# Performance work log

Hardware: AMD Instinct MI355X
Metric: run time of the kernel (lower is better)

The kernel has to match this reference:

```python
import jax, jax.numpy as jnp
import numpy as np

B, T, C = 8, 2048, 1024
HS = 128           # head_size
N_TERMS = 2
THETA = 10000.0


def _rope_tables(dim, end):
    freqs = 1.0 / (THETA ** (jnp.arange(0, dim, 2, dtype=jnp.float32) / dim))  # [dim/2]
    ang = jnp.arange(end, dtype=jnp.float32)[:, None] * freqs[None, :]          # [end, dim/2]
    return jnp.cos(ang), jnp.sin(ang)


def _apply_rope(x, cos, sin):
    # x: [..., T, D]; pairs are interleaved (x0,x1),(x2,x3),...
    xr = x[..., 0::2]
    xi = x[..., 1::2]
    or_ = xr * cos - xi * sin
    oi = xr * sin + xi * cos
    return jnp.stack([or_, oi], axis=-1).reshape(x.shape)


def setup_inputs() -> dict:
    key = jax.random.key(0)
    ks = jax.random.split(key, 6)
    x = jax.random.normal(ks[0], (B, T, C), dtype=jnp.float32)
    Wq = jax.random.normal(ks[1], (N_TERMS, C, HS), dtype=jnp.float32) * 0.02
    Wk = jax.random.normal(ks[2], (N_TERMS, C, HS), dtype=jnp.float32) * 0.02
    Wv = jax.random.normal(ks[3], (C, 2 * HS), dtype=jnp.float32) * 0.02
    lambda_q = jax.random.normal(ks[4], (N_TERMS, HS), dtype=jnp.float32) * 0.1
    lambda_k = jax.random.normal(ks[5], (N_TERMS, HS), dtype=jnp.float32) * 0.1
    return {"x": x, "Wq": Wq, "Wk": Wk, "Wv": Wv,
            "lambda_q": lambda_q, "lambda_k": lambda_k, "layer_idx": 3}


def reference(x, Wq, Wk, Wv, lambda_q, lambda_k, layer_idx):
    Bx, Tx, Cx = x.shape
    n = Wq.shape[0]
    scale = 1.0 / (HS ** 0.5)

    v = x @ Wv                                   # [B,T,2*HS]
    q = jnp.einsum('btc,ncd->nbtd', x, Wq)       # [n,B,T,HS]
    k = jnp.einsum('btc,ncd->nbtd', x, Wk)

    cos, sin = _rope_tables(HS, Tx)              # [T, HS/2]
    q = _apply_rope(q, cos, sin)
    k = _apply_rope(k, cos, sin)

    att = jnp.einsum('nbtd,nbsd->nbts', q, k) * scale  # [n,B,T,T]
    causal = jnp.tril(jnp.ones((Tx, Tx), dtype=bool))
    att = jnp.where(causal, att, -jnp.inf)
    att = jax.nn.softmax(att, axis=-1)

    # lambda values
    lam_init = 0.8 - 0.6 * jnp.exp(-0.3 * (jnp.float32(layer_idx) - 1.0))
    e = jnp.mean(jnp.exp(lambda_q * lambda_k), axis=-1)         # [n]
    e_prev = jnp.concatenate([jnp.zeros((1,), e.dtype), e[:-1]])
    lam = e - e_prev + lam_init                                 # [n]
    signs = jnp.where(jnp.arange(n) % 2 == 1, -1.0, 1.0)

    diff_att = jnp.einsum('n,nbts->bts', signs * lam, att)      # [B,T,T]
    out = diff_att @ v                                          # [B,T,2*HS]
    return out
```

## Files before the change

### kernel.cpp

```cpp
#include <hip/hip_runtime.h>
#include <math.h>

#define B_DIM 8
#define T_DIM 2048
#define C_DIM 1024
#define HS_DIM 128
#define VD 256
#define M_DIM (B_DIM * T_DIM)
#define QK_ELEMS (M_DIM * HS_DIM)
#define SCALE 0.088388347648318447f
#define LOG_THETA 9.210340371976184f

#define QB_OFF   0u
#define KB_OFF   4194304u
#define VT_OFF   8388608u
#define WT_OFF   12582912u
#define XBH_OFF  13369344u
#define LAM_OFF  21757952u
#define XSPLIT_ELEMS 8388608u

typedef short s8v   __attribute__((ext_vector_type(8)));
typedef float f32x4 __attribute__((ext_vector_type(4)));
typedef float f32x16 __attribute__((ext_vector_type(16)));

__device__ __forceinline__ unsigned int bf16_rne(float f) {
    unsigned int u = __float_as_uint(f);
    return (u + 0x7fffu + ((u >> 16) & 1u)) >> 16;
}
__device__ __forceinline__ unsigned int pack_bf2(float lo, float hi) {
    return bf16_rne(lo) | (bf16_rne(hi) << 16);
}
__device__ __forceinline__ void async_cp16(const unsigned short* g, unsigned short* l) {
    __builtin_amdgcn_global_load_lds(
        (const __attribute__((address_space(1))) unsigned int*)g,
        (__attribute__((address_space(3))) unsigned int*)l, 16, 0, 0);
}

__global__ __launch_bounds__(256) void prep_kernel(
    const float* __restrict__ x,
    const float* __restrict__ Wq, const float* __restrict__ Wk,
    const float* __restrict__ Wv,
    const float* __restrict__ lq, const float* __restrict__ lk,
    const int* __restrict__ lidx,
    unsigned short* __restrict__ xlo, unsigned short* __restrict__ xhi,
    unsigned short* __restrict__ wt, float* __restrict__ lam_out) {
    __shared__ float tile[32][33];
    const int bx = blockIdx.x;
    const int t = threadIdx.x;

    if (bx < 8192) {
        const size_t i8 = ((size_t)bx * 256 + t) * 8;
        float4 a = *(const float4*)(x + i8);
        float4 b = *(const float4*)(x + i8 + 4);
        uint4 u;
        u.x = pack_bf2(a.x, a.y); u.y = pack_bf2(a.z, a.w);
        u.z = pack_bf2(b.x, b.y); u.w = pack_bf2(b.z, b.w);
        unsigned short* dst = (i8 < XSPLIT_ELEMS) ? (xlo + i8) : (xhi + (i8 - XSPLIT_ELEMS));
        *(uint4*)dst = u;
    } else if (bx < 8960) {
        const int bxx = bx - 8192;
        const int n0 = (bxx % 24) * 32;
        const int k0 = (bxx / 24) * 32;
        const int seg = n0 >> 7;
        const int nl = t & 31;
        const int ng = n0 + nl;
        const int ngl = ng & 127;
        const int pcol = 2 * ((ngl & 15) + ((ngl >> 5) << 4)) + ((ngl >> 4) & 1);
        const float* src; int ld;
        if (seg < 2)      { src = Wq + (size_t)seg * (C_DIM * HS_DIM) + pcol; ld = 128; }
        else if (seg < 4) { src = Wk + (size_t)(seg - 2) * (C_DIM * HS_DIM) + pcol; ld = 128; }
        else              { src = Wv + (ng - 512); ld = 256; }
        #pragma unroll
        for (int rep = 0; rep < 4; ++rep) {
            int kl = (t >> 5) + rep * 8;
            tile[kl][nl] = src[(size_t)(k0 + kl) * ld];
        }
        __syncthreads();
        unsigned int* wt32 = (unsigned int*)wt;
        #pragma unroll
        for (int rep = 0; rep < 2; ++rep) {
            int nl2 = (t >> 4) + rep * 16;
            int k2 = (t & 15) * 2;
            unsigned int u = pack_bf2(tile[k2][nl2], tile[k2 + 1][nl2]);
            wt32[((size_t)(n0 + nl2) * 1024 + k0 + k2) >> 1] = u;
        }
    } else {
        if (t < 64) {
            float s0 = expf(lq[t] * lk[t]) + expf(lq[t + 64] * lk[t + 64]);
            float s1 = expf(lq[128 + t] * lk[128 + t]) + expf(lq[192 + t] * lk[192 + t]);
            #pragma unroll
            for (int off = 32; off > 0; off >>= 1) {
                s0 += __shfl_down(s0, off);
                s1 += __shfl_down(s1, off);
            }
            if (t == 0) {
                float e0 = s0 * (1.0f / 128.0f);
                float e1 = s1 * (1.0f / 128.0f);
                float li = 0.8f - 0.6f * expf(-0.3f * ((float)lidx[0] - 1.0f));
                lam_out[0] = e0 + li;
                lam_out[1] = -(e1 - e0 + li);
            }
        }
    }
}

__global__ __launch_bounds__(256) void gemm_kernel(
    const unsigned short* __restrict__ xlo, const unsigned short* __restrict__ xhi,
    const unsigned short* __restrict__ wt,
    unsigned short* __restrict__ qo, unsigned short* __restrict__ ko,
    unsigned short* __restrict__ vo) {
    __shared__ unsigned short AB[2][2][128 * 64];

    const int t = threadIdx.x;
    const int wv = t >> 6, lane = t & 63;
    const int quad = lane >> 4, l15 = lane & 15;
    const int m0 = blockIdx.x * 128;
    const int n0 = blockIdx.y * 128;
    const int wr = wv >> 1, wc = wv & 1;

    const unsigned short* xbase = (m0 < 8192)
        ? (xlo + (size_t)m0 * C_DIM) : (xhi + (size_t)(m0 - 8192) * C_DIM);
    const unsigned short* wbase = wt + (size_t)n0 * C_DIM;

    f32x4 acc[4][4];
    #pragma unroll
    for (int i = 0; i < 4; ++i)
        #pragma unroll
        for (int j = 0; j < 4; ++j) acc[i][j] = (f32x4){0.f, 0.f, 0.f, 0.f};

    int srow[4], sco[4];
    #pragma unroll
    for (int rep = 0; rep < 4; ++rep) {
        const int ci = t + rep * 256;
        srow[rep] = ci >> 3;
        sco[rep] = ((ci & 7) ^ (srow[rep] & 7)) * 8;
    }

    #pragma unroll
    for (int rep = 0; rep < 4; ++rep) {
        const int ci = t + rep * 256;
        async_cp16(xbase + (size_t)srow[rep] * C_DIM + sco[rep], &AB[0][0][ci * 8]);
        async_cp16(wbase + (size_t)srow[rep] * C_DIM + sco[rep], &AB[0][1][ci * 8]);
    }

    for (int it = 0; it < 16; ++it) {
        const int cur = it & 1;
        asm volatile("s_waitcnt vmcnt(0)" ::: "memory");
        __builtin_amdgcn_s_barrier();
        if (it + 1 < 16) {
            const int kn = (it + 1) * 64;
            #pragma unroll
            for (int rep = 0; rep < 4; ++rep) {
                const int ci = t + rep * 256;
                async_cp16(xbase + (size_t)srow[rep] * C_DIM + kn + sco[rep],
                           &AB[cur ^ 1][0][ci * 8]);
                async_cp16(wbase + (size_t)srow[rep] * C_DIM + kn + sco[rep],
                           &AB[cur ^ 1][1][ci * 8]);
            }
        }
        const unsigned short* As = AB[cur][0];
        const unsigned short* Bs = AB[cur][1];
        #pragma unroll
        for (int kk = 0; kk < 2; ++kk) {
            s8v af[4], bf[4];
            #pragma unroll
            for (int i = 0; i < 4; ++i) {
                const int row = wr * 64 + i * 16 + l15;
                const int xch = (kk * 4 + quad) ^ (row & 7);
                af[i] = *(const s8v*)&As[row * 64 + xch * 8];
            }
            #pragma unroll
            for (int j = 0; j < 4; ++j) {
                const int row = wc * 64 + j * 16 + l15;
                const int xch = (kk * 4 + quad) ^ (row & 7);
                bf[j] = *(const s8v*)&Bs[row * 64 + xch * 8];
            }
            #pragma unroll
            for (int i = 0; i < 4; ++i)
                #pragma unroll
                for (int j = 0; j < 4; ++j)
                    acc[i][j] = __builtin_amdgcn_mfma_f32_16x16x32_bf16(af[i], bf[j], acc[i][j], 0, 0, 0);
        }
    }

    const int seg = n0 >> 7;
    if (seg < 4) {
        unsigned short* dstbuf = ((seg < 2) ? qo : ko) + (size_t)(seg & 1) * QK_ELEMS;
        const int mi0 = l15 + 32 * wc;
        const int mi1 = mi0 + 16;
        const float freq0 = __expf((float)mi0 * (-LOG_THETA / 64.f));
        const float freq1 = __expf((float)mi1 * (-LOG_THETA / 64.f));
        #pragma unroll
        for (int i = 0; i < 4; ++i) {
            #pragma unroll
            for (int e = 0; e < 4; ++e) {
                const int m = m0 + wr * 64 + i * 16 + quad * 4 + e;
                const float trow = (float)(m & (T_DIM - 1));
                unsigned int* p32 = (unsigned int*)(dstbuf + (size_t)m * HS_DIM);
                float sn0, cs0, sn1, cs1;
                __sincosf(trow * freq0, &sn0, &cs0);
                __sincosf(trow * freq1, &sn1, &cs1);
                const float xr0 = acc[i][0][e], xi0 = acc[i][1][e];
                const float xr1 = acc[i][2][e], xi1 = acc[i][3][e];
                p32[mi0] = pack_bf2(xr0 * cs0 - xi0 * sn0, xr0 * sn0 + xi0 * cs0);
                p32[mi1] = pack_bf2(xr1 * cs1 - xi1 * sn1, xr1 * sn1 + xi1 * cs1);
            }
        }
    } else {
        const int bq = m0 >> 11;
        const int tbase = m0 & (T_DIM - 1);
        unsigned int* vT32 = (unsigned int*)vo;
        #pragma unroll
        for (int j = 0; j < 4; ++j) {
            const int d = (seg - 4) * 128 + wc * 64 + j * 16 + l15;
            const size_t rowbase = (size_t)(bq * VD + d) * (T_DIM / 2);
            #pragma unroll
            for (int i = 0; i < 4; ++i) {
                const int tok = tbase + wr * 64 + i * 16 + quad * 4;
                uint2 u;
                u.x = pack_bf2(acc[i][j][0], acc[i][j][1]);
                u.y = pack_bf2(acc[i][j][2], acc[i][j][3]);
                *(uint2*)&vT32[rowbase + (tok >> 1)] = u;
            }
        }
    }
}

#define PSTR 72
#define OSTR 260
#define BUFB 65536
#define P_OFF 131072
#define PSZ  9216
#define SM_TOTAL 149504

__global__ __launch_bounds__(512, 1) void attn_kernel(
    const unsigned short* __restrict__ qg, const unsigned short* __restrict__ kg,
    const unsigned short* __restrict__ vg, const float* __restrict__ lam,
    float* __restrict__ outp) {
    __shared__ __align__(16) unsigned char smem[SM_TOTAL];

    const int t = threadIdx.x;
    const int id = blockIdx.x;
    const int b = id & 7;
    const int kp = id >> 3;

    const int w = t >> 6, lane = t & 63;
    const int l31 = lane & 31, lh = lane >> 5;
    const int sg = w >> 2;
    const int term = w & 1;
    const int kh = (w >> 1) & 1;

    const int strip = sg ? kp : (63 - kp);
    const int q0 = strip * 32;
    const int ntS = (strip >> 1) + 1;
    const int ntB = ((63 - kp) >> 1) + 1;

    unsigned short* Ps = (unsigned short*)(smem + P_OFF + sg * PSZ);
    float* Lsum = (float*)(smem + P_OFF + sg * PSZ);
    float* Ol = (float*)(smem + sg * BUFB);

    const float cn = lam[term];

    const unsigned short* qrow = qg
        + ((size_t)(term * B_DIM + b) * T_DIM + q0 + l31) * HS_DIM + lh * 8;
    s8v qa[8];
    #pragma unroll
    for (int ks = 0; ks < 8; ++ks)
        qa[ks] = *(const s8v*)(qrow + ks * 16);

    unsigned int kOffA[4], vOffA[4];
    #pragma unroll
    for (int rep = 0; rep < 4; ++rep) {
        const int c = t + rep * 512;
        const int rowg = c >> 4, slot = c & 15;
        const int kterm = rowg >> 6, krow = rowg & 63;
        const int kss = slot ^ (krow & 15);
        kOffA[rep] = (unsigned int)(((kterm * B_DIM + b) * T_DIM + krow) * HS_DIM
                                    + kss * 8);
        const int drow = rowg;
        const int vss = slot ^ (drow & 15);
        const int dim = 2 * drow + (vss >> 3), tokc = vss & 7;
        vOffA[rep] = (unsigned int)((b * VD + dim) * T_DIM + tokc * 8);
    }

    f32x16 o[4];
    #pragma unroll
    for (int dt = 0; dt < 4; ++dt)
        #pragma unroll
        for (int r = 0; r < 16; ++r) o[dt][r] = 0.f;
    float l_acc[16];
    #pragma unroll
    for (int r = 0; r < 16; ++r) l_acc[r] = 0.f;

    {
        unsigned short* kb0 = (unsigned short*)(smem + w * 1024);
        unsigned short* vb0 = (unsigned short*)(smem + 32768 + w * 1024);
        #pragma unroll
        for (int rep = 0; rep < 4; ++rep) {
            async_cp16(kg + kOffA[rep], kb0 + rep * 4096);
            async_cp16(vg + vOffA[rep], vb0 + rep * 4096);
        }
    }
    __syncthreads();

    const int krow = kh * 32 + l31;
    const int k15 = l31 & 15;

    for (int it = 0; it < ntB; ++it) {
        const int s0 = it * 64;
        const unsigned char* buf = smem + (it & 1) * BUFB;

        if (it + 1 < ntB) {
            const int sn = s0 + 64;
            unsigned char* nbuf = smem + ((it + 1) & 1) * BUFB;
            unsigned short* kbn = (unsigned short*)(nbuf + w * 1024);
            unsigned short* vbn = (unsigned short*)(nbuf + 32768 + w * 1024);
            #pragma unroll
            for (int rep = 0; rep < 4; ++rep) {
                async_cp16(kg + kOffA[rep] + (size_t)sn * HS_DIM, kbn + rep * 4096);
                async_cp16(vg + vOffA[rep] + sn, vbn + rep * 4096);
            }
        }

        if (it < ntS) {
            const unsigned short* Kb = (const unsigned short*)buf;
            f32x16 sc;
            #pragma unroll
            for (int r = 0; r < 16; ++r) sc[r] = 0.f;
            __builtin_amdgcn_s_setprio(1);
            #pragma unroll
            for (int ks = 0; ks < 8; ++ks) {
                const int x = (ks * 2 + lh) ^ k15;
                s8v kf = *(const s8v*)&Kb[(term * 64 + krow) * 128 + x * 8];
                sc = __builtin_amdgcn_mfma_f32_32x32x16_bf16(qa[ks], kf, sc, 0, 0, 0);
            }
            __builtin_amdgcn_s_setprio(0);
            const int key = s0 + kh * 32 + l31;
            #pragma unroll
            for (int r = 0; r < 16; ++r) {
                const int row = (r & 3) + 8 * (r >> 2) + 4 * lh;
                const float p = (key <= q0 + row) ? __expf(sc[r] * SCALE) : 0.f;
                l_acc[r] += p;
                Ps[(term * 32 + row) * PSTR + kh * 32 + l31] = (unsigned short)bf16_rne(p);
            }
        }
        asm volatile("s_waitcnt lgkmcnt(0)\n\ts_barrier" ::: "memory");
        __builtin_amdgcn_sched_barrier(0);

        if (it < ntS) {
            const unsigned short* Vb = (const unsigned short*)(buf + 32768);
            __builtin_amdgcn_s_setprio(1);
            #pragma unroll
            for (int ks = 0; ks < 4; ++ks) {
                s8v pa = *(const s8v*)&Ps[(term * 32 + l31) * PSTR + ks * 16 + lh * 8];
                #pragma unroll
                for (int dt = 0; dt < 4; ++dt) {
                    const int dim = kh * 128 + dt * 32 + l31;
                    const int drow = dim >> 1;
                    const int x = ((dim & 1) * 8 + ks * 2 + lh) ^ (drow & 15);
                    s8v vb = *(const s8v*)&Vb[(drow * 16 + x) * 8];
                    o[dt] = __builtin_amdgcn_mfma_f32_32x32x16_bf16(pa, vb, o[dt], 0, 0, 0);
                }
            }
            __builtin_amdgcn_s_setprio(0);
        }
        __syncthreads();
    }

    #pragma unroll
    for (int r = 0; r < 16; ++r) {
        float lt = l_acc[r];
        #pragma unroll
        for (int off = 1; off < 32; off <<= 1) lt += __shfl_xor(lt, off);
        if (l31 == 0) {
            const int row = (r & 3) + 8 * (r >> 2) + 4 * lh;
            Lsum[(term * 2 + kh) * 32 + row] = lt;
        }
    }
    __syncthreads();
    float inv[16];
    #pragma unroll
    for (int r = 0; r < 16; ++r) {
        const int row = (r & 3) + 8 * (r >> 2) + 4 * lh;
        inv[r] = cn / (Lsum[(term * 2 + 0) * 32 + row] + Lsum[(term * 2 + 1) * 32 + row]);
    }

    if (term) {
        #pragma unroll
        for (int dt = 0; dt < 4; ++dt)
            #pragma unroll
            for (int r = 0; r < 16; ++r) {
                const int row = (r & 3) + 8 * (r >> 2) + 4 * lh;
                Ol[row * OSTR + kh * 128 + dt * 32 + l31] = o[dt][r] * inv[r];
            }
    }
    __syncthreads();
    if (!term) {
        #pragma unroll
        for (int dt = 0; dt < 4; ++dt)
            #pragma unroll
            for (int r = 0; r < 16; ++r) {
                const int row = (r & 3) + 8 * (r >> 2) + 4 * lh;
                Ol[row * OSTR + kh * 128 + dt * 32 + l31] += o[dt][r] * inv[r];
            }
    }
    __syncthreads();
    #pragma unroll
    for (int rep = 0; rep < 8; ++rep) {
        int idx = (t & 255) + rep * 256;
        int row = idx >> 6, c4 = idx & 63;
        float4 val = *(const float4*)&Ol[row * OSTR + c4 * 4];
        *(float4*)&outp[((size_t)(b * T_DIM + q0 + row)) * VD + c4 * 4] = val;
    }
}

extern "C" void kernel_launch(void* const* d_in, const int* in_sizes, int n_in,
                              void* d_out, int out_size, void* d_ws, size_t ws_size,
                              hipStream_t stream) {
    const float* x  = (const float*)d_in[0];
    const float* Wq = (const float*)d_in[1];
    const float* Wk = (const float*)d_in[2];
    const float* Wv = (const float*)d_in[3];
    const float* lq = (const float*)d_in[4];
    const float* lk = (const float*)d_in[5];
    const int* lidx = (const int*)d_in[6];

    unsigned short* ws = (unsigned short*)d_ws;
    unsigned short* qb   = ws + QB_OFF;
    unsigned short* kb   = ws + KB_OFF;
    unsigned short* vTb  = ws + VT_OFF;
    unsigned short* wtb  = ws + WT_OFF;
    unsigned short* xbhi = ws + XBH_OFF;
    float* lamb = (float*)(ws + LAM_OFF);
    unsigned short* xblo = (unsigned short*)d_out;
    (void)ws_size; (void)in_sizes; (void)n_in; (void)out_size;

    prep_kernel<<<dim3(8961), dim3(256), 0, stream>>>(
        x, Wq, Wk, Wv, lq, lk, lidx, xblo, xbhi, wtb, lamb);
    gemm_kernel<<<dim3(128, 6), dim3(256), 0, stream>>>(xblo, xbhi, wtb, qb, kb, vTb);
    attn_kernel<<<dim3(256), dim3(512), 0, stream>>>(qb, kb, vTb, lamb, (float*)d_out);
}
```

Measured before the change: 200.5 us.

## Fuse prep, projection GEMM and attention into one persistent kernel with grid barriers

Replaces the three launches (prep, GEMM, attention) with a single persistent 256-block kernel. Phases are separated by software grid barriers built on an atomic counter that is cleared with a memset before launch. The intent is to remove launch gaps and tail effects between the kernels. In exchange, the GEMM now runs as 512 half-block tiles in two rounds, with some tiles left idle. Correctness also depends on all 256 blocks being resident at once, since otherwise the spin barrier can deadlock.

```diff
diff --git a/kernel.cpp b/kernel.cpp
--- a/kernel.cpp
+++ b/kernel.cpp
@@ -17,11 +17,19 @@
 #define WT_OFF   12582912u
 #define XBH_OFF  13369344u
 #define LAM_OFF  21757952u
+#define BAR_OFF  21757960u
 #define XSPLIT_ELEMS 8388608u
 
 typedef short s8v   __attribute__((ext_vector_type(8)));
 typedef float f32x4 __attribute__((ext_vector_type(4)));
 typedef float f32x16 __attribute__((ext_vector_type(16)));
+
+#define PSTR 72
+#define OSTR 260
+#define BUFB 65536
+#define P_OFF 131072
+#define PSZ  9216
+#define SM_TOTAL 149504
 
 __device__ __forceinline__ unsigned int bf16_rne(float f) {
     unsigned int u = __float_as_uint(f);
@@ -35,382 +43,400 @@
         (const __attribute__((address_space(1))) unsigned int*)g,
         (__attribute__((address_space(3))) unsigned int*)l, 16, 0, 0);
 }
-
-__global__ __launch_bounds__(256) void prep_kernel(
+__device__ __forceinline__ void grid_barrier(unsigned int* ctr) {
+    __syncthreads();
+    if (threadIdx.x == 0) {
+        __atomic_fetch_add(ctr, 1u, __ATOMIC_ACQ_REL);
+        while (__atomic_load_n(ctr, __ATOMIC_ACQUIRE) < 256u)
+            __builtin_amdgcn_s_sleep(16);
+    }
+    __syncthreads();
+}
+
+__global__ __launch_bounds__(512, 1) void mega_kernel(
     const float* __restrict__ x,
     const float* __restrict__ Wq, const float* __restrict__ Wk,
     const float* __restrict__ Wv,
     const float* __restrict__ lq, const float* __restrict__ lk,
     const int* __restrict__ lidx,
     unsigned short* __restrict__ xlo, unsigned short* __restrict__ xhi,
-    unsigned short* __restrict__ wt, float* __restrict__ lam_out) {
-    __shared__ float tile[32][33];
-    const int bx = blockIdx.x;
+    unsigned short* __restrict__ wt, float* __restrict__ lamb,
+    unsigned short* __restrict__ qb, unsigned short* __restrict__ kb,
+    unsigned short* __restrict__ vT, float* __restrict__ outp,
+    unsigned int* __restrict__ bar) {
+    __shared__ __align__(16) unsigned char smem[SM_TOTAL];
+
     const int t = threadIdx.x;
-
-    if (bx < 8192) {
-        const size_t i8 = ((size_t)bx * 256 + t) * 8;
-        float4 a = *(const float4*)(x + i8);
-        float4 b = *(const float4*)(x + i8 + 4);
-        uint4 u;
-        u.x = pack_bf2(a.x, a.y); u.y = pack_bf2(a.z, a.w);
-        u.z = pack_bf2(b.x, b.y); u.w = pack_bf2(b.z, b.w);
-        unsigned short* dst = (i8 < XSPLIT_ELEMS) ? (xlo + i8) : (xhi + (i8 - XSPLIT_ELEMS));
-        *(uint4*)dst = u;
-    } else if (bx < 8960) {
-        const int bxx = bx - 8192;
-        const int n0 = (bxx % 24) * 32;
-        const int k0 = (bxx / 24) * 32;
-        const int seg = n0 >> 7;
-        const int nl = t & 31;
-        const int ng = n0 + nl;
-        const int ngl = ng & 127;
-        const int pcol = 2 * ((ngl & 15) + ((ngl >> 5) << 4)) + ((ngl >> 4) & 1);
-        const float* src; int ld;
-        if (seg < 2)      { src = Wq + (size_t)seg * (C_DIM * HS_DIM) + pcol; ld = 128; }
-        else if (seg < 4) { src = Wk + (size_t)(seg - 2) * (C_DIM * HS_DIM) + pcol; ld = 128; }
-        else              { src = Wv + (ng - 512); ld = 256; }
+    const int bid = blockIdx.x;
+
+    {
+        const int idx = bid * 512 + t;
+        #pragma unroll 4
+        for (int iter = 0; iter < 16; ++iter) {
+            const size_t i8 = (size_t)(idx + (iter << 17)) * 8;
+            float4 a = *(const float4*)(x + i8);
+            float4 b = *(const float4*)(x + i8 + 4);
+            uint4 u;
+            u.x = pack_bf2(a.x, a.y); u.y = pack_bf2(a.z, a.w);
+            u.z = pack_bf2(b.x, b.y); u.w = pack_bf2(b.z, b.w);
+            unsigned short* dst = (i8 < XSPLIT_ELEMS) ? (xlo + i8)
+                                                      : (xhi + (i8 - XSPLIT_ELEMS));
+            *(uint4*)dst = u;
+        }
+    }
+    {
+        float (*tile)[33] = (float(*)[33])smem;
+        for (int r = 0; r < 3; ++r) {
+            const int bxx = bid + (r << 8);
+            const int n0 = (bxx % 24) * 32;
+            const int k0 = (bxx / 24) * 32;
+            const int seg = n0 >> 7;
+            const int nl = t & 31;
+            const int ng = n0 + nl;
+            const int ngl = ng & 127;
+            const int pcol = 2 * ((ngl & 15) + ((ngl >> 5) << 4)) + ((ngl >> 4) & 1);
+            const float* src; int ld;
+            if (seg < 2)      { src = Wq + (size_t)seg * (C_DIM * HS_DIM) + pcol; ld = 128; }
+            else if (seg < 4) { src = Wk + (size_t)(seg - 2) * (C_DIM * HS_DIM) + pcol; ld = 128; }
+            else              { src = Wv + (ng - 512); ld = 256; }
+            #pragma unroll
+            for (int rep = 0; rep < 2; ++rep) {
+                int kl = (t >> 5) + rep * 16;
+                tile[kl][nl] = src[(size_t)(k0 + kl) * ld];
+            }
+            __syncthreads();
+            unsigned int* wt32 = (unsigned int*)wt;
+            {
+                int nl2 = t >> 4;
+                int k2 = (t & 15) * 2;
+                unsigned int u = pack_bf2(tile[k2][nl2], tile[k2 + 1][nl2]);
+                wt32[((size_t)(n0 + nl2) * 1024 + k0 + k2) >> 1] = u;
+            }
+            __syncthreads();
+        }
+    }
+    if (bid == 0 && t < 64) {
+        float s0 = expf(lq[t] * lk[t]) + expf(lq[t + 64] * lk[t + 64]);
+        float s1 = expf(lq[128 + t] * lk[128 + t]) + expf(lq[192 + t] * lk[192 + t]);
+        #pragma unroll
+        for (int off = 32; off > 0; off >>= 1) {
+            s0 += __shfl_down(s0, off);
+            s1 += __shfl_down(s1, off);
+        }
+        if (t == 0) {
+            float e0 = s0 * (1.0f / 128.0f);
+            float e1 = s1 * (1.0f / 128.0f);
+            float li = 0.8f - 0.6f * expf(-0.3f * ((float)lidx[0] - 1.0f));
+            lamb[0] = e0 + li;
+            lamb[1] = -(e1 - e0 + li);
+        }
+    }
+    grid_barrier(bar + 0);
+
+    {
+        const int half = t >> 8, th = t & 255;
+        const int wv = th >> 6, lane = th & 63;
+        const int quad = lane >> 4, l15 = lane & 15;
+        const int wr = wv >> 1, wc = wv & 1;
+        unsigned short* AB = (unsigned short*)(smem + half * 65536);
+
+        int srow[4], sco[4];
         #pragma unroll
         for (int rep = 0; rep < 4; ++rep) {
-            int kl = (t >> 5) + rep * 8;
-            tile[kl][nl] = src[(size_t)(k0 + kl) * ld];
+            const int ci = th + rep * 256;
+            srow[rep] = ci >> 3;
+            sco[rep] = ((ci & 7) ^ (srow[rep] & 7)) * 8;
+        }
+
+        #pragma unroll 1
+        for (int r = 0; r < 2; ++r) {
+            const int tile = bid * 2 + half + (r << 9);
+            const bool active = tile < 768;
+            const int m0 = (tile & 127) * 128;
+            const int n0 = (tile >> 7) * 128;
+            const unsigned short* xbase = (m0 < 8192)
+                ? (xlo + (size_t)m0 * C_DIM) : (xhi + (size_t)(m0 - 8192) * C_DIM);
+            const unsigned short* wbase = wt + (size_t)n0 * C_DIM;
+
+            f32x4 acc[4][4];
+            #pragma unroll
+            for (int i = 0; i < 4; ++i)
+                #pragma unroll
+                for (int j = 0; j < 4; ++j) acc[i][j] = (f32x4){0.f, 0.f, 0.f, 0.f};
+
+            if (active) {
+                #pragma unroll
+                for (int rep = 0; rep < 4; ++rep) {
+                    const int ci = th + rep * 256;
+                    async_cp16(xbase + (size_t)srow[rep] * C_DIM + sco[rep], AB + ci * 8);
+                    async_cp16(wbase + (size_t)srow[rep] * C_DIM + sco[rep], AB + 8192 + ci * 8);
+                }
+            }
+            for (int it = 0; it < 16; ++it) {
+                const int cur = it & 1;
+                asm volatile("s_waitcnt vmcnt(0)" ::: "memory");
+                __builtin_amdgcn_s_barrier();
+                if (active && it + 1 < 16) {
+                    const int kn = (it + 1) * 64;
+                    const int nb = (cur ^ 1) * 2;
+                    #pragma unroll
+                    for (int rep = 0; rep < 4; ++rep) {
+                        const int ci = th + rep * 256;
+                        async_cp16(xbase + (size_t)srow[rep] * C_DIM + kn + sco[rep],
+                                   AB + nb * 8192 + ci * 8);
+                        async_cp16(wbase + (size_t)srow[rep] * C_DIM + kn + sco[rep],
+                                   AB + (nb + 1) * 8192 + ci * 8);
+                    }
+                }
+                if (active) {
+                    const unsigned short* As = AB + cur * 16384;
+                    const unsigned short* Bs = AB + cur * 16384 + 8192;
+                    #pragma unroll
+                    for (int kk = 0; kk < 2; ++kk) {
+                        s8v af[4], bf[4];
+                        #pragma unroll
+                        for (int i = 0; i < 4; ++i) {
+                            const int row = wr * 64 + i * 16 + l15;
+                            const int xch = (kk * 4 + quad) ^ (row & 7);
+                            af[i] = *(const s8v*)&As[row * 64 + xch * 8];
+                        }
+                        #pragma unroll
+                        for (int j = 0; j < 4; ++j) {
+                            const int row = wc * 64 + j * 16 + l15;
+                            const int xch = (kk * 4 + quad) ^ (row & 7);
+                            bf[j] = *(const s8v*)&Bs[row * 64 + xch * 8];
+                        }
+                        #pragma unroll
+                        for (int i = 0; i < 4; ++i)
+                            #pragma unroll
+                            for (int j = 0; j < 4; ++j)
+                                acc[i][j] = __builtin_amdgcn_mfma_f32_16x16x32_bf16(
+                                    af[i], bf[j], acc[i][j], 0, 0, 0);
+                    }
+                }
+            }
+            if (active) {
+                const int seg = n0 >> 7;
+                if (seg < 4) {
+                    unsigned short* dstbuf = ((seg < 2) ? qb : kb)
+                        + (size_t)(seg & 1) * QK_ELEMS;
+                    const int mi0 = l15 + 32 * wc;
+                    const int mi1 = mi0 + 16;
+                    const float freq0 = __expf((float)mi0 * (-LOG_THETA / 64.f));
+                    const float freq1 = __expf((float)mi1 * (-LOG_THETA / 64.f));
+                    #pragma unroll
+                    for (int i = 0; i < 4; ++i) {
+                        #pragma unroll
+                        for (int e = 0; e < 4; ++e) {
+                            const int m = m0 + wr * 64 + i * 16 + quad * 4 + e;
+                            const float trow = (float)(m & (T_DIM - 1));
+                            unsigned int* p32 = (unsigned int*)(dstbuf + (size_t)m * HS_DIM);
+                            float sn0, cs0, sn1, cs1;
+                            __sincosf(trow * freq0, &sn0, &cs0);
+                            __sincosf(trow * freq1, &sn1, &cs1);
+                            const float xr0 = acc[i][0][e], xi0 = acc[i][1][e];
+                            const float xr1 = acc[i][2][e], xi1 = acc[i][3][e];
+                            p32[mi0] = pack_bf2(xr0 * cs0 - xi0 * sn0, xr0 * sn0 + xi0 * cs0);
+                            p32[mi1] = pack_bf2(xr1 * cs1 - xi1 * sn1, xr1 * sn1 + xi1 * cs1);
+                        }
+                    }
+                } else {
+                    const int bq = m0 >> 11;
+                    const int tbase = m0 & (T_DIM - 1);
+                    unsigned int* vT32 = (unsigned int*)vT;
+                    #pragma unroll
+                    for (int j = 0; j < 4; ++j) {
+                        const int d = (seg - 4) * 128 + wc * 64 + j * 16 + l15;
+                        const size_t rowbase = (size_t)(bq * VD + d) * (T_DIM / 2);
+                        #pragma unroll
+                        for (int i = 0; i < 4; ++i) {
+                            const int tok = tbase + wr * 64 + i * 16 + quad * 4;
+                            uint2 u;
+                            u.x = pack_bf2(acc[i][j][0], acc[i][j][1]);
+                            u.y = pack_bf2(acc[i][j][2], acc[i][j][3]);
+                            *(uint2*)&vT32[rowbase + (tok >> 1)] = u;
+                        }
+                    }
+                }
+            }
+            __syncthreads();
+        }
+    }
+    grid_barrier(bar + 1);
+
+    {
+        const int id = bid;
+        const int b = id & 7;
+        const int kp = id >> 3;
+
+        const int w = t >> 6, lane = t & 63;
+        const int l31 = lane & 31, lh = lane >> 5;
+        const int sg = w >> 2;
+        const int term = w & 1;
+        const int kh = (w >> 1) & 1;
+
+        const int strip = sg ? kp : (63 - kp);
+        const int q0 = strip * 32;
+        const int ntS = (strip >> 1) + 1;
+        const int ntB = ((63 - kp) >> 1) + 1;
+
+        unsigned short* Ps = (unsigned short*)(smem + P_OFF + sg * PSZ);
+        float* Lsum = (float*)(smem + P_OFF + sg * PSZ);
+        float* Ol = (float*)(smem + sg * BUFB);
+
+        const float cn = lamb[term];
+
+        const unsigned short* qrow = qb
+            + ((size_t)(term * B_DIM + b) * T_DIM + q0 + l31) * HS_DIM + lh * 8;
+        s8v qa[8];
+        #pragma unroll
+        for (int ks = 0; ks < 8; ++ks)
+            qa[ks] = *(const s8v*)(qrow + ks * 16);
+
+        unsigned int kOffA[4], vOffA[4];
+        #pragma unroll
+        for (int rep = 0; rep < 4; ++rep) {
+            const int c = t + rep * 512;
+            const int rowg = c >> 4, slot = c & 15;
+            const int kterm = rowg >> 6, krw = rowg & 63;
+            const int kss = slot ^ (krw & 15);
+            kOffA[rep] = (unsigned int)(((kterm * B_DIM + b) * T_DIM + krw) * HS_DIM
+                                        + kss * 8);
+            const int drow = rowg;
+            const int vss = slot ^ (drow & 15);
+            const int dim = 2 * drow + (vss >> 3), tokc = vss & 7;
+            vOffA[rep] = (unsigned int)((b * VD + dim) * T_DIM + tokc * 8);
+        }
+
+        f32x16 o[4];
+        #pragma unroll
+        for (int dt = 0; dt < 4; ++dt)
+            #pragma unroll
+            for (int r = 0; r < 16; ++r) o[dt][r] = 0.f;
+        float l_acc[16];
+        #pragma unroll
+        for (int r = 0; r < 16; ++r) l_acc[r] = 0.f;
+
+        {
+            unsigned short* kb0 = (unsigned short*)(smem + w * 1024);
+            unsigned short* vb0 = (unsigned short*)(smem + 32768 + w * 1024);
+            #pragma unroll
+            for (int rep = 0; rep < 4; ++rep) {
+                async_cp16(kb + kOffA[rep], kb0 + rep * 4096);
+                async_cp16(vT + vOffA[rep], vb0 + rep * 4096);
+            }
         }
         __syncthreads();
-        unsigned int* wt32 = (unsigned int*)wt;
-        #pragma unroll
-        for (int rep = 0; rep < 2; ++rep) {
-            int nl2 = (t >> 4) + rep * 16;
-            int k2 = (t & 15) * 2;
-            unsigned int u = pack_bf2(tile[k2][nl2], tile[k2 + 1][nl2]);
-            wt32[((size_t)(n0 + nl2) * 1024 + k0 + k2) >> 1] = u;
-        }
-    } else {
-        if (t < 64) {
-            float s0 = expf(lq[t] * lk[t]) + expf(lq[t + 64] * lk[t + 64]);
-            float s1 = expf(lq[128 + t] * lk[128 + t]) + expf(lq[192 + t] * lk[192 + t]);
-            #pragma unroll
-            for (int off = 32; off > 0; off >>= 1) {
-                s0 += __shfl_down(s0, off);
-                s1 += __shfl_down(s1, off);
-            }
-            if (t == 0) {
-                float e0 = s0 * (1.0f / 128.0f);
-                float e1 = s1 * (1.0f / 128.0f);
-                float li = 0.8f - 0.6f * expf(-0.3f * ((float)lidx[0] - 1.0f));
-                lam_out[0] = e0 + li;
-                lam_out[1] = -(e1 - e0 + li);
-            }
-        }
-    }
-}
-
-__global__ __launch_bounds__(256) void gemm_kernel(
-    const unsigned short* __restrict__ xlo, const unsigned short* __restrict__ xhi,
-    const unsigned short* __restrict__ wt,
-    unsigned short* __restrict__ qo, unsigned short* __restrict__ ko,
-    unsigned short* __restrict__ vo) {
-    __shared__ unsigned short AB[2][2][128 * 64];
-
-    const int t = threadIdx.x;
-    const int wv = t >> 6, lane = t & 63;
-    const int quad = lane >> 4, l15 = lane & 15;
-    const int m0 = blockIdx.x * 128;
-    const int n0 = blockIdx.y * 128;
-    const int wr = wv >> 1, wc = wv & 1;
-
-    const unsigned short* xbase = (m0 < 8192)
-        ? (xlo + (size_t)m0 * C_DIM) : (xhi + (size_t)(m0 - 8192) * C_DIM);
-    const unsigned short* wbase = wt + (size_t)n0 * C_DIM;
-
-    f32x4 acc[4][4];
-    #pragma unroll
-    for (int i = 0; i < 4; ++i)
-        #pragma unroll
-        for (int j = 0; j < 4; ++j) acc[i][j] = (f32x4){0.f, 0.f, 0.f, 0.f};
-
-    int srow[4], sco[4];
-    #pragma unroll
-    for (int rep = 0; rep < 4; ++rep) {
-        const int ci = t + rep * 256;
-        srow[rep] = ci >> 3;
-        sco[rep] = ((ci & 7) ^ (srow[rep] & 7)) * 8;
-    }
-
-    #pragma unroll
-    for (int rep = 0; rep < 4; ++rep) {
-        const int ci = t + rep * 256;
-        async_cp16(xbase + (size_t)srow[rep] * C_DIM + sco[rep], &AB[0][0][ci * 8]);
-        async_cp16(wbase + (size_t)srow[rep] * C_DIM + sco[rep], &AB[0][1][ci * 8]);
-    }
-
-    for (int it = 0; it < 16; ++it) {
-        const int cur = it & 1;
-        asm volatile("s_waitcnt vmcnt(0)" ::: "memory");
-        __builtin_amdgcn_s_barrier();
-        if (it + 1 < 16) {
-            const int kn = (it + 1) * 64;
-            #pragma unroll
-            for (int rep = 0; rep < 4; ++rep) {
-                const int ci = t + rep * 256;
-                async_cp16(xbase + (size_t)srow[rep] * C_DIM + kn + sco[rep],
-                           &AB[cur ^ 1][0][ci * 8]);
-                async_cp16(wbase + (size_t)srow[rep] * C_DIM + kn + sco[rep],
-                           &AB[cur ^ 1][1][ci * 8]);
-            }
-        }
-        const unsigned short* As = AB[cur][0];
-        const unsigned short* Bs = AB[cur][1];
-        #pragma unroll
-        for (int kk = 0; kk < 2; ++kk) {
-            s8v af[4], bf[4];
-            #pragma unroll
-            for (int i = 0; i < 4; ++i) {
-                const int row = wr * 64 + i * 16 + l15;
-                const int xch = (kk * 4 + quad) ^ (row & 7);
-                af[i] = *(const s8v*)&As[row * 64 + xch * 8];
-            }
-            #pragma unroll
-            for (int j = 0; j < 4; ++j) {
-                const int row = wc * 64 + j * 16 + l15;
-                const int xch = (kk * 4 + quad) ^ (row & 7);
-                bf[j] = *(const s8v*)&Bs[row * 64 + xch * 8];
-            }
-            #pragma unroll
-            for (int i = 0; i < 4; ++i)
-                #pragma unroll
-                for (int j = 0; j < 4; ++j)
-                    acc[i][j] = __builtin_amdgcn_mfma_f32_16x16x32_bf16(af[i], bf[j], acc[i][j], 0, 0, 0);
-        }
-    }
-
-    const int seg = n0 >> 7;
-    if (seg < 4) {
-        unsigned short* dstbuf = ((seg < 2) ? qo : ko) + (size_t)(seg & 1) * QK_ELEMS;
-        const int mi0 = l15 + 32 * wc;
-        const int mi1 = mi0 + 16;
-        const float freq0 = __expf((float)mi0 * (-LOG_THETA / 64.f));
-        const float freq1 = __expf((float)mi1 * (-LOG_THETA / 64.f));
-        #pragma unroll
-        for (int i = 0; i < 4; ++i) {
-            #pragma unroll
-            for (int e = 0; e < 4; ++e) {
-                const int m = m0 + wr * 64 + i * 16 + quad * 4 + e;
-                const float trow = (float)(m & (T_DIM - 1));
-                unsigned int* p32 = (unsigned int*)(dstbuf + (size_t)m * HS_DIM);
-                float sn0, cs0, sn1, cs1;
-                __sincosf(trow * freq0, &sn0, &cs0);
-                __sincosf(trow * freq1, &sn1, &cs1);
-                const float xr0 = acc[i][0][e], xi0 = acc[i][1][e];
-                const float xr1 = acc[i][2][e], xi1 = acc[i][3][e];
-                p32[mi0] = pack_bf2(xr0 * cs0 - xi0 * sn0, xr0 * sn0 + xi0 * cs0);
-                p32[mi1] = pack_bf2(xr1 * cs1 - xi1 * sn1, xr1 * sn1 + xi1 * cs1);
-            }
-        }
-    } else {
-        const int bq = m0 >> 11;
-        const int tbase = m0 & (T_DIM - 1);
-        unsigned int* vT32 = (unsigned int*)vo;
-        #pragma unroll
-        for (int j = 0; j < 4; ++j) {
-            const int d = (seg - 4) * 128 + wc * 64 + j * 16 + l15;
-            const size_t rowbase = (size_t)(bq * VD + d) * (T_DIM / 2);
-            #pragma unroll
-            for (int i = 0; i < 4; ++i) {
-                const int tok = tbase + wr * 64 + i * 16 + quad * 4;
-                uint2 u;
-                u.x = pack_bf2(acc[i][j][0], acc[i][j][1]);
-                u.y = pack_bf2(acc[i][j][2], acc[i][j][3]);
-                *(uint2*)&vT32[rowbase + (tok >> 1)] = u;
-            }
-        }
-    }
-}
-
-#define PSTR 72
-#define OSTR 260
-#define BUFB 65536
-#define P_OFF 131072
-#define PSZ  9216
-#define SM_TOTAL 149504
-
-__global__ __launch_bounds__(512, 1) void attn_kernel(
-    const unsigned short* __restrict__ qg, const unsigned short* __restrict__ kg,
-    const unsigned short* __restrict__ vg, const float* __restrict__ lam,
-    float* __restrict__ outp) {
-    __shared__ __align__(16) unsigned char smem[SM_TOTAL];
-
-    const int t = threadIdx.x;
-    const int id = blockIdx.x;
-    const int b = id & 7;
-    const int kp = id >> 3;
-
-    const int w = t >> 6, lane = t & 63;
-    const int l31 = lane & 31, lh = lane >> 5;
-    const int sg = w >> 2;
-    const int term = w & 1;
-    const int kh = (w >> 1) & 1;
-
-    const int strip = sg ? kp : (63 - kp);
-    const int q0 = strip * 32;
-    const int ntS = (strip >> 1) + 1;
-    const int ntB = ((63 - kp) >> 1) + 1;
-
-    unsigned short* Ps = (unsigned short*)(smem + P_OFF + sg * PSZ);
-    float* Lsum = (float*)(smem + P_OFF + sg * PSZ);
-    float* Ol = (float*)(smem + sg * BUFB);
-
-    const float cn = lam[term];
-
-    const unsigned short* qrow = qg
-        + ((size_t)(term * B_DIM + b) * T_DIM + q0 + l31) * HS_DIM + lh * 8;
-    s8v qa[8];
-    #pragma unroll
-    for (int ks = 0; ks < 8; ++ks)
-        qa[ks] = *(const s8v*)(qrow + ks * 16);
-
-    unsigned int kOffA[4], vOffA[4];
-    #pragma unroll
-    for (int rep = 0; rep < 4; ++rep) {
-        const int c = t + rep * 512;
-        const int rowg = c >> 4, slot = c & 15;
-        const int kterm = rowg >> 6, krow = rowg & 63;
-        const int kss = slot ^ (krow & 15);
-        kOffA[rep] = (unsigned int)(((kterm * B_DIM + b) * T_DIM + krow) * HS_DIM
-                                    + kss * 8);
-        const int drow = rowg;
-        const int vss = slot ^ (drow & 15);
-        const int dim = 2 * drow + (vss >> 3), tokc = vss & 7;
-        vOffA[rep] = (unsigned int)((b * VD + dim) * T_DIM + tokc * 8);
-    }
-
-    f32x16 o[4];
-    #pragma unroll
-    for (int dt = 0; dt < 4; ++dt)
-        #pragma unroll
-        for (int r = 0; r < 16; ++r) o[dt][r] = 0.f;
-    float l_acc[16];
-    #pragma unroll
-    for (int r = 0; r < 16; ++r) l_acc[r] = 0.f;
-
-    {
-        unsigned short* kb0 = (unsigned short*)(smem + w * 1024);
-        unsigned short* vb0 = (unsigned short*)(smem + 32768 + w * 1024);
-        #pragma unroll
-        for (int rep = 0; rep < 4; ++rep) {
-            async_cp16(kg + kOffA[rep], kb0 + rep * 4096);
-            async_cp16(vg + vOffA[rep], vb0 + rep * 4096);
-        }
-    }
-    __syncthreads();
-
-    const int krow = kh * 32 + l31;
-    const int k15 = l31 & 15;
-
-    for (int it = 0; it < ntB; ++it) {
-        const int s0 = it * 64;
-        const unsigned char* buf = smem + (it & 1) * BUFB;
-
-        if (it + 1 < ntB) {
-            const int sn = s0 + 64;
-            unsigned char* nbuf = smem + ((it + 1) & 1) * BUFB;
-            unsigned short* kbn = (unsigned short*)(nbuf + w * 1024);
-            unsigned short* vbn = (unsigned short*)(nbuf + 32768 + w * 1024);
-            #pragma unroll
-            for (int rep = 0; rep < 4; ++rep) {
-                async_cp16(kg + kOffA[rep] + (size_t)sn * HS_DIM, kbn + rep * 4096);
-                async_cp16(vg + vOffA[rep] + sn, vbn + rep * 4096);
-            }
-        }
-
-        if (it < ntS) {
-            const unsigned short* Kb = (const unsigned short*)buf;
-            f32x16 sc;
-            #pragma unroll
-            for (int r = 0; r < 16; ++r) sc[r] = 0.f;
-            __builtin_amdgcn_s_setprio(1);
-            #pragma unroll
-            for (int ks = 0; ks < 8; ++ks) {
-                const int x = (ks * 2 + lh) ^ k15;
-                s8v kf = *(const s8v*)&Kb[(term * 64 + krow) * 128 + x * 8];
-                sc = __builtin_amdgcn_mfma_f32_32x32x16_bf16(qa[ks], kf, sc, 0, 0, 0);
-            }
-            __builtin_amdgcn_s_setprio(0);
-            const int key = s0 + kh * 32 + l31;
-            #pragma unroll
-            for (int r = 0; r < 16; ++r) {
+
+        const int krow = kh * 32 + l31;
+        const int k15 = l31 & 15;
+
+        for (int it = 0; it < ntB; ++it) {
+            const int s0 = it * 64;
+            const unsigned char* buf = smem + (it & 1) * BUFB;
+
+            if (it + 1 < ntB) {
+                const int sn = s0 + 64;
+                unsigned char* nbuf = smem + ((it + 1) & 1) * BUFB;
+                unsigned short* kbn = (unsigned short*)(nbuf + w * 1024);
+                unsigned short* vbn = (unsigned short*)(nbuf + 32768 + w * 1024);
+                #pragma unroll
+                for (int rep = 0; rep < 4; ++rep) {
+                    async_cp16(kb + kOffA[rep] + (size_t)sn * HS_DIM, kbn + rep * 4096);
+                    async_cp16(vT + vOffA[rep] + sn, vbn + rep * 4096);
+                }
+            }
+
+            if (it < ntS) {
+                const unsigned short* Kb = (const unsigned short*)buf;
+                f32x16 sc;
+                #pragma unroll
+                for (int r = 0; r < 16; ++r) sc[r] = 0.f;
+                __builtin_amdgcn_s_setprio(1);
+                #pragma unroll
+                for (int ks = 0; ks < 8; ++ks) {
+                    const int xx = (ks * 2 + lh) ^ k15;
+                    s8v kf = *(const s8v*)&Kb[(term * 64 + krow) * 128 + xx * 8];
+                    sc = __builtin_amdgcn_mfma_f32_32x32x16_bf16(qa[ks], kf, sc, 0, 0, 0);
+                }
+                __builtin_amdgcn_s_setprio(0);
+                const int key = s0 + kh * 32 + l31;
+                #pragma unroll
+                for (int r = 0; r < 16; ++r) {
+                    const int row = (r & 3) + 8 * (r >> 2) + 4 * lh;
+                    const float p = (key <= q0 + row) ? __expf(sc[r] * SCALE) : 0.f;
+                    l_acc[r] += p;
+                    Ps[(term * 32 + row) * PSTR + kh * 32 + l31] = (unsigned short)bf16_rne(p);
+                }
+            }
+            asm volatile("s_waitcnt lgkmcnt(0)\n\ts_barrier" ::: "memory");
+            __builtin_amdgcn_sched_barrier(0);
+
+            if (it < ntS) {
+                const unsigned short* Vb = (const unsigned short*)(buf + 32768);
+                __builtin_amdgcn_s_setprio(1);
+                #pragma unroll
+                for (int ks = 0; ks < 4; ++ks) {
+                    s8v pa = *(const s8v*)&Ps[(term * 32 + l31) * PSTR + ks * 16 + lh * 8];
+                    #pragma unroll
+                    for (int dt = 0; dt < 4; ++dt) {
+                        const int dim = kh * 128 + dt * 32 + l31;
+                        const int drow = dim >> 1;
+                        const int xx = ((dim & 1) * 8 + ks * 2 + lh) ^ (drow & 15);
+                        s8v vb = *(const s8v*)&Vb[(drow * 16 + xx) * 8];
+                        o[dt] = __builtin_amdgcn_mfma_f32_32x32x16_bf16(pa, vb, o[dt], 0, 0, 0);
+                    }
+                }
+                __builtin_amdgcn_s_setprio(0);
+            }
+            __syncthreads();
+        }
+
+        #pragma unroll
+        for (int r = 0; r < 16; ++r) {
+            float lt = l_acc[r];
+            #pragma unroll
+            for (int off = 1; off < 32; off <<= 1) lt += __shfl_xor(lt, off);
+            if (l31 == 0) {
                 const int row = (r & 3) + 8 * (r >> 2) + 4 * lh;
-                const float p = (key <= q0 + row) ? __expf(sc[r] * SCALE) : 0.f;
-                l_acc[r] += p;
-                Ps[(term * 32 + row) * PSTR + kh * 32 + l31] = (unsigned short)bf16_rne(p);
-            }
-        }
-        asm volatile("s_waitcnt lgkmcnt(0)\n\ts_barrier" ::: "memory");
-        __builtin_amdgcn_sched_barrier(0);
-
-        if (it < ntS) {
-            const unsigned short* Vb = (const unsigned short*)(buf + 32768);
-            __builtin_amdgcn_s_setprio(1);
-            #pragma unroll
-            for (int ks = 0; ks < 4; ++ks) {
-                s8v pa = *(const s8v*)&Ps[(term * 32 + l31) * PSTR + ks * 16 + lh * 8];
-                #pragma unroll
-                for (int dt = 0; dt < 4; ++dt) {
-                    const int dim = kh * 128 + dt * 32 + l31;
-                    const int drow = dim >> 1;
-                    const int x = ((dim & 1) * 8 + ks * 2 + lh) ^ (drow & 15);
-                    s8v vb = *(const s8v*)&Vb[(drow * 16 + x) * 8];
-                    o[dt] = __builtin_amdgcn_mfma_f32_32x32x16_bf16(pa, vb, o[dt], 0, 0, 0);
-                }
-            }
-            __builtin_amdgcn_s_setprio(0);
+                Lsum[(term * 2 + kh) * 32 + row] = lt;
+            }
         }
         __syncthreads();
-    }
-
-    #pragma unroll
-    for (int r = 0; r < 16; ++r) {
-        float lt = l_acc[r];
-        #pragma unroll
-        for (int off = 1; off < 32; off <<= 1) lt += __shfl_xor(lt, off);
-        if (l31 == 0) {
+        float inv[16];
+        #pragma unroll
+        for (int r = 0; r < 16; ++r) {
             const int row = (r & 3) + 8 * (r >> 2) + 4 * lh;
-            Lsum[(term * 2 + kh) * 32 + row] = lt;
-        }
-    }
-    __syncthreads();
-    float inv[16];
-    #pragma unroll
-    for (int r = 0; r < 16; ++r) {
-        const int row = (r & 3) + 8 * (r >> 2) + 4 * lh;
-        inv[r] = cn / (Lsum[(term * 2 + 0) * 32 + row] + Lsum[(term * 2 + 1) * 32 + row]);
-    }
-
-    if (term) {
-        #pragma unroll
-        for (int dt = 0; dt < 4; ++dt)
-            #pragma unroll
-            for (int r = 0; r < 16; ++r) {
-                const int row = (r & 3) + 8 * (r >> 2) + 4 * lh;
-                Ol[row * OSTR + kh * 128 + dt * 32 + l31] = o[dt][r] * inv[r];
-            }
-    }
-    __syncthreads();
-    if (!term) {
-        #pragma unroll
-        for (int dt = 0; dt < 4; ++dt)
-            #pragma unroll
-            for (int r = 0; r < 16; ++r) {
-                const int row = (r & 3) + 8 * (r >> 2) + 4 * lh;
-                Ol[row * OSTR + kh * 128 + dt * 32 + l31] += o[dt][r] * inv[r];
-            }
-    }
-    __syncthreads();
-    #pragma unroll
-    for (int rep = 0; rep < 8; ++rep) {
-        int idx = (t & 255) + rep * 256;
-        int row = idx >> 6, c4 = idx & 63;
-        float4 val = *(const float4*)&Ol[row * OSTR + c4 * 4];
-        *(float4*)&outp[((size_t)(b * T_DIM + q0 + row)) * VD + c4 * 4] = val;
+            inv[r] = cn / (Lsum[(term * 2 + 0) * 32 + row] + Lsum[(term * 2 + 1) * 32 + row]);
+        }
+
+        if (term) {
+            #pragma unroll
+            for (int dt = 0; dt < 4; ++dt)
+                #pragma unroll
+                for (int r = 0; r < 16; ++r) {
+                    const int row = (r & 3) + 8 * (r >> 2) + 4 * lh;
+                    Ol[row * OSTR + kh * 128 + dt * 32 + l31] = o[dt][r] * inv[r];
+                }
+        }
+        __syncthreads();
+        if (!term) {
+            #pragma unroll
+            for (int dt = 0; dt < 4; ++dt)
+                #pragma unroll
+                for (int r = 0; r < 16; ++r) {
+                    const int row = (r & 3) + 8 * (r >> 2) + 4 * lh;
+                    Ol[row * OSTR + kh * 128 + dt * 32 + l31] += o[dt][r] * inv[r];
+                }
+        }
+        __syncthreads();
+        #pragma unroll
+        for (int rep = 0; rep < 8; ++rep) {
+            int idx = (t & 255) + rep * 256;
+            int row = idx >> 6, c4 = idx & 63;
+            float4 val = *(const float4*)&Ol[row * OSTR + c4 * 4];
+            *(float4*)&outp[((size_t)(b * T_DIM + q0 + row)) * VD + c4 * 4] = val;
+        }
     }
 }
 
@@ -432,11 +458,12 @@
     unsigned short* wtb  = ws + WT_OFF;
     unsigned short* xbhi = ws + XBH_OFF;
     float* lamb = (float*)(ws + LAM_OFF);
+    unsigned int* barb = (unsigned int*)(ws + BAR_OFF);
     unsigned short* xblo = (unsigned short*)d_out;
     (void)ws_size; (void)in_sizes; (void)n_in; (void)out_size;
 
-    prep_kernel<<<dim3(8961), dim3(256), 0, stream>>>(
-        x, Wq, Wk, Wv, lq, lk, lidx, xblo, xbhi, wtb, lamb);
-    gemm_kernel<<<dim3(128, 6), dim3(256), 0, stream>>>(xblo, xbhi, wtb, qb, kb, vTb);
-    attn_kernel<<<dim3(256), dim3(512), 0, stream>>>(qb, kb, vTb, lamb, (float*)d_out);
-}
+    hipMemsetAsync(barb, 0, 8, stream);
+    mega_kernel<<<dim3(256), dim3(512), 0, stream>>>(
+        x, Wq, Wk, Wv, lq, lk, lidx, xblo, xbhi, wtb, lamb,
+        qb, kb, vTb, (float*)d_out, barb);
+}
```

After: 280.1 us. 1.4x slower.
